# Performance work log

Hardware: AMD Instinct MI355X
Metric: run time of the kernel (lower is better)

The kernel has to match this reference:

```python
import jax, jax.numpy as jnp
import numpy as np

N_NODES = 100000
N_EDGES = 1600000
NEG_SLOPE = 0.2  # PyG GATConv default


def setup_inputs() -> dict:
    key = jax.random.key(0)
    ks = jax.random.split(key, 10)
    return {
        "x": jax.random.normal(ks[0], (N_NODES, 128), dtype=jnp.float32),
        "edge_index": jax.random.randint(ks[1], (2, N_EDGES), 0, N_NODES, dtype=jnp.int64),
        "W1": jax.random.normal(ks[2], (128, 128), dtype=jnp.float32) * 0.1,
        "a_src1": jax.random.normal(ks[3], (4, 32), dtype=jnp.float32) * 0.1,
        "a_dst1": jax.random.normal(ks[4], (4, 32), dtype=jnp.float32) * 0.1,
        "b1": jax.random.normal(ks[5], (128,), dtype=jnp.float32) * 0.1,
        "W2": jax.random.normal(ks[6], (128, 16), dtype=jnp.float32) * 0.1,
        "a_src2": jax.random.normal(ks[7], (1, 16), dtype=jnp.float32) * 0.1,
        "a_dst2": jax.random.normal(ks[8], (1, 16), dtype=jnp.float32) * 0.1,
        "b2": jax.random.normal(ks[9], (16,), dtype=jnp.float32) * 0.1,
    }


def _gat_layer(x, src, dst, W, a_src, a_dst, b, heads):
    # PyG GATConv (concat=True): xw -> per-edge attention -> segment softmax over
    # incoming edges of each target node -> weighted scatter-sum.
    N = x.shape[0]
    H = heads
    C = W.shape[1] // H
    xw = (x @ W).reshape(N, H, C)                      # [N,H,C]
    al = (xw * a_src).sum(-1)                          # [N,H] source term
    ar = (xw * a_dst).sum(-1)                          # [N,H] target term
    e = jax.nn.leaky_relu(al[src] + ar[dst], NEG_SLOPE)  # [E',H]
    emax = jax.ops.segment_max(e, dst, num_segments=N)   # [N,H]
    em = jnp.exp(e - emax[dst])
    denom = jax.ops.segment_sum(em, dst, num_segments=N)
    alpha = em / denom[dst]                            # [E',H]
    out = jax.ops.segment_sum(xw[src] * alpha[:, :, None], dst, num_segments=N)
    return out.reshape(N, H * C) + b


def reference(x, edge_index, W1, a_src1, a_dst1, b1, W2, a_src2, a_dst2, b2):
    N = x.shape[0]
    loop = jnp.arange(N, dtype=edge_index.dtype)
    # PyG GATConv add_self_loops=True
    src = jnp.concatenate([edge_index[0], loop])
    dst = jnp.concatenate([edge_index[1], loop])
    h = jax.nn.relu(_gat_layer(x, src, dst, W1, a_src1, a_dst1, b1, 4))
    # F.dropout(p=0.5, training=self.training): identity in eval mode
    return _gat_layer(h, src, dst, W2, a_src2, a_dst2, b2, 1)
```

## Files before the change

kernel.cpp:

```cpp
#include <hip/hip_runtime.h>
#include <hip/hip_fp16.h>

#define N_NODES 100000
#define N_EDGES 1600000
#define E_TOT   (N_EDGES + N_NODES)
#define NEG_SLOPE 0.2f
#define PART_EPB 4096
#define BSTRIDE 18432

__global__ __launch_bounds__(256)
void k_part(const int* __restrict__ ei, int* __restrict__ bcnt, int* __restrict__ pairs) {
    const int t = threadIdx.x;
    const int base = blockIdx.x * PART_EPB;
    __shared__ int lcnt[128];
    __shared__ int lbase[128];
    if (t < 128) lcnt[t] = 0;
    __syncthreads();
    int sr[16], dr[16];
#pragma unroll
    for (int u = 0; u < 16; ++u) {
        const int e = base + u * 256 + t;
        if (e < E_TOT) {
            int s, d;
            if (e < N_EDGES) { s = ei[e]; d = ei[N_EDGES + e]; }
            else             { s = d = e - N_EDGES; }
            sr[u] = s; dr[u] = d;
            atomicAdd(&lcnt[d >> 10], 1);
        } else dr[u] = -1;
    }
    __syncthreads();
    if (t < 128) {
        const int c = lcnt[t];
        lbase[t] = (c > 0) ? atomicAdd(&bcnt[t], c) : 0;
        lcnt[t] = 0;
    }
    __syncthreads();
#pragma unroll
    for (int u = 0; u < 16; ++u) {
        if (dr[u] >= 0) {
            const int bk = dr[u] >> 10;
            const int r = atomicAdd(&lcnt[bk], 1);
            pairs[(size_t)bk * BSTRIDE + lbase[bk] + r] = (sr[u] << 10) | (dr[u] & 1023);
        }
    }
}

__global__ __launch_bounds__(1024)
void k_fill3(const int* __restrict__ pairs, const int* __restrict__ bcnt,
             int* __restrict__ ioff, int* __restrict__ deg, int* __restrict__ ssrc) {
    const int bucket = blockIdx.x;
    const int t = threadIdx.x;
    const int cnt = bcnt[bucket];
    __shared__ int lhist[1024];
    __shared__ int lcur[1024];
    __shared__ int wsum[16];
    __shared__ int sbase;
    lhist[t] = 0;
    if (t == 0) {
        int b = 0;
        for (int k = 0; k < bucket; ++k) b += bcnt[k];
        sbase = b;
    }
    __syncthreads();
    for (int i = t; i < cnt; i += 1024) {
        const int p = pairs[(size_t)bucket * BSTRIDE + i];
        atomicAdd(&lhist[p & 1023], 1);
    }
    __syncthreads();
    const int v = lhist[t];
    int inc = v;
    const int lane = t & 63, wid = t >> 6;
#pragma unroll
    for (int o = 1; o < 64; o <<= 1) {
        const int nv = __shfl_up(inc, o, 64);
        if (lane >= o) inc += nv;
    }
    if (lane == 63) wsum[wid] = inc;
    __syncthreads();
    if (t == 0) {
        int acc = 0;
#pragma unroll
        for (int k = 0; k < 16; ++k) { const int tv = wsum[k]; wsum[k] = acc; acc += tv; }
    }
    __syncthreads();
    const int gofs = sbase + (inc - v) + wsum[wid];
    const int d = bucket * 1024 + t;
    if (d < N_NODES) { ioff[d] = gofs; deg[d] = v; }
    lcur[t] = gofs;
    __syncthreads();
    for (int i = t; i < cnt; i += 1024) {
        const int p = pairs[(size_t)bucket * BSTRIDE + i];
        const int pos = atomicAdd(&lcur[p & 1023], 1);
        ssrc[pos] = p >> 10;
    }
}

__global__ __launch_bounds__(256)
void k_gemm1(const float* __restrict__ x, const float* __restrict__ W1,
             const float* __restrict__ a_src1, const float* __restrict__ a_dst1,
             __half* __restrict__ xw1h, float* __restrict__ al1, float* __restrict__ ar1) {
    const int t = threadIdx.x;
    const int n0 = blockIdx.x * 32;
    __shared__ float sx[32][128];
    __shared__ float sW[32][128];

    {
        const float4* xg = (const float4*)(x + (size_t)n0 * 128);
#pragma unroll
        for (int i = 0; i < 4; ++i) {
            const int f = t + i * 256;
            ((float4*)sx)[f] = xg[f];
        }
    }

    const int tj = t & 31;
    const int tn = (t >> 5) * 4;
    float4 acc[4] = {{0,0,0,0},{0,0,0,0},{0,0,0,0},{0,0,0,0}};

    for (int kt = 0; kt < 128; kt += 32) {
        __syncthreads();
        const float4* wg = (const float4*)(W1 + (size_t)kt * 128);
#pragma unroll
        for (int i = 0; i < 4; ++i) {
            const int f = t + i * 256;
            ((float4*)sW)[f] = wg[f];
        }
        __syncthreads();
        for (int k = 0; k < 32; k += 4) {
            float4 xv[4];
#pragma unroll
            for (int i = 0; i < 4; ++i)
                xv[i] = *(const float4*)&sx[tn + i][kt + k];
#pragma unroll
            for (int kk = 0; kk < 4; ++kk) {
                const float4 wv = *(const float4*)&sW[k + kk][tj * 4];
#pragma unroll
                for (int i = 0; i < 4; ++i) {
                    const float xs = ((const float*)&xv[i])[kk];
                    acc[i].x = fmaf(xs, wv.x, acc[i].x);
                    acc[i].y = fmaf(xs, wv.y, acc[i].y);
                    acc[i].z = fmaf(xs, wv.z, acc[i].z);
                    acc[i].w = fmaf(xs, wv.w, acc[i].w);
                }
            }
        }
    }

#pragma unroll
    for (int i = 0; i < 4; ++i) {
        __half hp[4];
        hp[0] = __float2half(acc[i].x);
        hp[1] = __float2half(acc[i].y);
        hp[2] = __float2half(acc[i].z);
        hp[3] = __float2half(acc[i].w);
        *(uint2*)&xw1h[(size_t)(n0 + tn + i) * 128 + tj * 4] = *(uint2*)hp;
    }

    const float4 asv = ((const float4*)a_src1)[tj];
    const float4 adv = ((const float4*)a_dst1)[tj];
#pragma unroll
    for (int i = 0; i < 4; ++i) {
        float ps = acc[i].x * asv.x + acc[i].y * asv.y + acc[i].z * asv.z + acc[i].w * asv.w;
        float pd = acc[i].x * adv.x + acc[i].y * adv.y + acc[i].z * adv.z + acc[i].w * adv.w;
#pragma unroll
        for (int o = 1; o < 8; o <<= 1) { ps += __shfl_xor(ps, o, 64); pd += __shfl_xor(pd, o, 64); }
        if ((tj & 7) == 0) {
            const int h = tj >> 3;
            al1[(size_t)(n0 + tn + i) * 4 + h] = ps;
            ar1[(size_t)(n0 + tn + i) * 4 + h] = pd;
        }
    }
}

__global__ __launch_bounds__(256)
void k_aggr1(const int* __restrict__ ssrc, const int* __restrict__ offs,
             const int* __restrict__ deg, const float* __restrict__ al1,
             const float* __restrict__ ar1, const __half* __restrict__ xw1h,
             const float* __restrict__ b1, __half* __restrict__ out1h) {
    const int lane = threadIdx.x & 63;
    const int d = blockIdx.x * 4 + (threadIdx.x >> 6);
    const int g = lane >> 4;
    const int c = lane & 15;
    const int h = c >> 2;
    const int beg = offs[d];
    const int n = deg[d];
    const float arh = ar1[(size_t)d * 4 + h];
    float acc[8] = {0.f, 0.f, 0.f, 0.f, 0.f, 0.f, 0.f, 0.f};
    float dnm = 0.f;

    for (int base = 0; base < n; base += 8) {
#pragma unroll
        for (int u = 0; u < 2; ++u) {
            const int e = base + u * 4 + g;
            const bool p = e < n;
            const int s = ssrc[beg + (p ? e : 0)];
            float v = al1[(size_t)s * 4 + h] + arh;
            v = v > 0.f ? v : NEG_SLOPE * v;
            const float w = p ? __expf(v) : 0.f;
            const uint4 rv = *(const uint4*)&xw1h[(size_t)s * 128 + c * 8];
            const float2 f0 = __half22float2(*(const __half2*)&rv.x);
            const float2 f1 = __half22float2(*(const __half2*)&rv.y);
            const float2 f2 = __half22float2(*(const __half2*)&rv.z);
            const float2 f3 = __half22float2(*(const __half2*)&rv.w);
            acc[0] = fmaf(w, f0.x, acc[0]); acc[1] = fmaf(w, f0.y, acc[1]);
            acc[2] = fmaf(w, f1.x, acc[2]); acc[3] = fmaf(w, f1.y, acc[3]);
            acc[4] = fmaf(w, f2.x, acc[4]); acc[5] = fmaf(w, f2.y, acc[5]);
            acc[6] = fmaf(w, f3.x, acc[6]); acc[7] = fmaf(w, f3.y, acc[7]);
            dnm += w;
        }
    }
#pragma unroll
    for (int i = 0; i < 8; ++i) {
        acc[i] += __shfl_xor(acc[i], 16, 64);
        acc[i] += __shfl_xor(acc[i], 32, 64);
    }
    dnm += __shfl_xor(dnm, 16, 64);
    dnm += __shfl_xor(dnm, 32, 64);
    if (g == 0) {
        const float rc = 1.f / dnm;
        const float4 b01 = *(const float4*)&b1[c * 8];
        const float4 b23 = *(const float4*)&b1[c * 8 + 4];
        const float bb[8] = {b01.x, b01.y, b01.z, b01.w, b23.x, b23.y, b23.z, b23.w};
        __half ho[8];
#pragma unroll
        for (int i = 0; i < 8; ++i) {
            const float hv = acc[i] * rc + bb[i];
            ho[i] = __float2half(hv > 0.f ? hv : 0.f);
        }
        *(uint4*)&out1h[(size_t)d * 128 + c * 8] = *(uint4*)ho;
    }
}

__global__ __launch_bounds__(256)
void k_gemm2(const __half* __restrict__ out1h, const float* __restrict__ W2,
             const float* __restrict__ a_src2, const float* __restrict__ a_dst2,
             __half* __restrict__ xw2h, float* __restrict__ al2, float* __restrict__ ar2) {
    const int t = threadIdx.x;
    const int node0 = blockIdx.x * 16;
    __shared__ float sW[128 * 16];
    __shared__ float sh[16][129];
    for (int i = t; i < 2048; i += 256) sW[i] = W2[i];
    for (int i = t; i < 2048; i += 256) {
        const int nn = i >> 7, kk = i & 127;
        sh[nn][kk] = __half2float(out1h[(size_t)(node0 + nn) * 128 + kk]);
    }
    __syncthreads();
    const int nn = t >> 4;
    const int j = t & 15;
    float acc = 0.f;
#pragma unroll 8
    for (int k = 0; k < 128; ++k)
        acc = fmaf(sh[nn][k], sW[k * 16 + j], acc);
    xw2h[(size_t)(node0 + nn) * 16 + j] = __float2half(acc);

    float ps = acc * a_src2[j];
    float pd = acc * a_dst2[j];
#pragma unroll
    for (int o = 8; o; o >>= 1) { ps += __shfl_xor(ps, o, 64); pd += __shfl_xor(pd, o, 64); }
    if (j == 0) { al2[node0 + nn] = ps; ar2[node0 + nn] = pd; }
}

__global__ __launch_bounds__(256)
void k_aggr2(const int* __restrict__ ssrc, const int* __restrict__ offs,
             const int* __restrict__ deg, const float* __restrict__ al2,
             const float* __restrict__ ar2, const __half* __restrict__ xw2h,
             const float* __restrict__ b2, float* __restrict__ out) {
    const int lane = threadIdx.x & 63;
    const int node = blockIdx.x * 4 + (threadIdx.x >> 6);
    const int j2 = lane & 7;
    const int eL = lane >> 3;
    const int beg = offs[node];
    const int n = deg[node];
    const float ard = ar2[node];
    float a0 = 0.f, a1 = 0.f, dnm = 0.f;
    for (int base = 0; base < n; base += 16) {
#pragma unroll
        for (int u = 0; u < 2; ++u) {
            const int e = base + u * 8 + eL;
            const bool p = e < n;
            const int s = ssrc[beg + (p ? e : 0)];
            float v = al2[s] + ard;
            v = v > 0.f ? v : NEG_SLOPE * v;
            const float w = p ? __expf(v) : 0.f;
            const float2 f = __half22float2(*(const __half2*)&xw2h[(size_t)s * 16 + j2 * 2]);
            a0 = fmaf(w, f.x, a0);
            a1 = fmaf(w, f.y, a1);
            dnm += w;
        }
    }
#pragma unroll
    for (int o = 8; o < 64; o <<= 1) {
        a0 += __shfl_xor(a0, o, 64);
        a1 += __shfl_xor(a1, o, 64);
        dnm += __shfl_xor(dnm, o, 64);
    }
    if (eL == 0) {
        out[(size_t)node * 16 + j2 * 2]     = a0 / dnm + b2[j2 * 2];
        out[(size_t)node * 16 + j2 * 2 + 1] = a1 / dnm + b2[j2 * 2 + 1];
    }
}

extern "C" void kernel_launch(void* const* d_in, const int* in_sizes, int n_in,
                              void* d_out, int out_size, void* d_ws, size_t ws_size,
                              hipStream_t stream) {
    const float* x      = (const float*)d_in[0];
    const int*   ei     = (const int*)d_in[1];
    const float* W1     = (const float*)d_in[2];
    const float* a_src1 = (const float*)d_in[3];
    const float* a_dst1 = (const float*)d_in[4];
    const float* b1     = (const float*)d_in[5];
    const float* W2     = (const float*)d_in[6];
    const float* a_src2 = (const float*)d_in[7];
    const float* a_dst2 = (const float*)d_in[8];
    const float* b2     = (const float*)d_in[9];
    float* out = (float*)d_out;

    char* wsb = (char*)d_ws;
    __half* xw1h = (__half*)wsb;
    __half* xw2h = (__half*)wsb;
    float*  al2  = (float*)(wsb + (size_t)N_NODES * 16 * 2);
    float*  ar2  = al2 + N_NODES;
    __half* out1h = (__half*)(wsb + (size_t)N_NODES * 128 * 2);
    int*    pairs = (int*)out1h;
    float*  al1  = (float*)(wsb + (size_t)N_NODES * 128 * 4);
    float*  ar1  = al1 + (size_t)N_NODES * 4;
    int* ibcnt = (int*)(ar1 + (size_t)N_NODES * 4);
    int* ioff  = ibcnt + 128;
    int* ideg  = ioff + N_NODES;
    int* isrc  = ideg + N_NODES;

    hipMemsetAsync(ibcnt, 0, 128 * sizeof(int), stream);

    k_part<<<(E_TOT + PART_EPB - 1) / PART_EPB, 256, 0, stream>>>(ei, ibcnt, pairs);
    k_fill3<<<128, 1024, 0, stream>>>(pairs, ibcnt, ioff, ideg, isrc);

    k_gemm1<<<N_NODES / 32, 256, 0, stream>>>(x, W1, a_src1, a_dst1, xw1h, al1, ar1);
    k_aggr1<<<N_NODES / 4, 256, 0, stream>>>(isrc, ioff, ideg, al1, ar1, xw1h, b1, out1h);

    k_gemm2<<<N_NODES / 16, 256, 0, stream>>>(out1h, W2, a_src2, a_dst2, xw2h, al2, ar2);
    k_aggr2<<<N_NODES / 4, 256, 0, stream>>>(isrc, ioff, ideg, al2, ar2, xw2h, b2, out);
}
```

Baseline: 355.4 us.

## Fuse layer-1 GEMM with edge partitioning and use fp16 MFMA

Merges the edge-partition kernel and the layer-1 projection GEMM into one launch, with block ranges split between the two tasks so they run side by side. The GEMM moves from an LDS-tiled fp32 FMA loop to fp16 MFMA 16x16x32 instructions, loading x and W1 straight from global memory and converting them to half in registers. This removes a kernel launch and the FMA-bound GEMM time, but rounds the GEMM inputs to fp16 and reads W1 with strided scalar loads.

```diff
diff --git a/kernel.cpp b/kernel.cpp
--- a/kernel.cpp
+++ b/kernel.cpp
@@ -7,40 +7,119 @@
 #define NEG_SLOPE 0.2f
 #define PART_EPB 4096
 #define BSTRIDE 18432
+#define NGEMM (N_NODES / 32)
+#define NPART ((E_TOT + PART_EPB - 1) / PART_EPB)
+
+using f16x8 = __attribute__((ext_vector_type(8))) _Float16;
+using f32x4 = __attribute__((ext_vector_type(4))) float;
+union H8 { f16x8 v; _Float16 h[8]; };
 
 __global__ __launch_bounds__(256)
-void k_part(const int* __restrict__ ei, int* __restrict__ bcnt, int* __restrict__ pairs) {
-    const int t = threadIdx.x;
-    const int base = blockIdx.x * PART_EPB;
+void k_gemm1_part(const float* __restrict__ x, const float* __restrict__ W1,
+                  const float* __restrict__ a_src1, const float* __restrict__ a_dst1,
+                  const int* __restrict__ ei, int* __restrict__ bcnt, int* __restrict__ pairs,
+                  __half* __restrict__ xw1h, float* __restrict__ al1, float* __restrict__ ar1) {
     __shared__ int lcnt[128];
     __shared__ int lbase[128];
-    if (t < 128) lcnt[t] = 0;
-    __syncthreads();
-    int sr[16], dr[16];
-#pragma unroll
-    for (int u = 0; u < 16; ++u) {
-        const int e = base + u * 256 + t;
-        if (e < E_TOT) {
-            int s, d;
-            if (e < N_EDGES) { s = ei[e]; d = ei[N_EDGES + e]; }
-            else             { s = d = e - N_EDGES; }
-            sr[u] = s; dr[u] = d;
-            atomicAdd(&lcnt[d >> 10], 1);
-        } else dr[u] = -1;
-    }
-    __syncthreads();
-    if (t < 128) {
-        const int c = lcnt[t];
-        lbase[t] = (c > 0) ? atomicAdd(&bcnt[t], c) : 0;
-        lcnt[t] = 0;
-    }
-    __syncthreads();
-#pragma unroll
-    for (int u = 0; u < 16; ++u) {
-        if (dr[u] >= 0) {
-            const int bk = dr[u] >> 10;
-            const int r = atomicAdd(&lcnt[bk], 1);
-            pairs[(size_t)bk * BSTRIDE + lbase[bk] + r] = (sr[u] << 10) | (dr[u] & 1023);
+    const int t = threadIdx.x;
+
+    if (blockIdx.x >= NGEMM) {
+        const int base = ((int)blockIdx.x - NGEMM) * PART_EPB;
+        if (t < 128) lcnt[t] = 0;
+        __syncthreads();
+        int sr[16], dr[16];
+#pragma unroll
+        for (int u = 0; u < 16; ++u) {
+            const int e = base + u * 256 + t;
+            if (e < E_TOT) {
+                int s, d;
+                if (e < N_EDGES) { s = ei[e]; d = ei[N_EDGES + e]; }
+                else             { s = d = e - N_EDGES; }
+                sr[u] = s; dr[u] = d;
+                atomicAdd(&lcnt[d >> 10], 1);
+            } else dr[u] = -1;
+        }
+        __syncthreads();
+        if (t < 128) {
+            const int c = lcnt[t];
+            lbase[t] = (c > 0) ? atomicAdd(&bcnt[t], c) : 0;
+            lcnt[t] = 0;
+        }
+        __syncthreads();
+#pragma unroll
+        for (int u = 0; u < 16; ++u) {
+            if (dr[u] >= 0) {
+                const int bk = dr[u] >> 10;
+                const int r = atomicAdd(&lcnt[bk], 1);
+                pairs[(size_t)bk * BSTRIDE + lbase[bk] + r] = (sr[u] << 10) | (dr[u] & 1023);
+            }
+        }
+        return;
+    }
+
+    const int lane = t & 63;
+    const int w = t >> 6;
+    const int q = lane >> 4;
+    const int n15 = lane & 15;
+    const int n0 = (int)blockIdx.x * 32;
+    const int j0 = (2 * w) * 16 + n15;
+    const int j1 = (2 * w + 1) * 16 + n15;
+
+    f32x4 acc00 = {0.f, 0.f, 0.f, 0.f};
+    f32x4 acc01 = acc00, acc10 = acc00, acc11 = acc00;
+
+    for (int kt = 0; kt < 4; ++kt) {
+        const int k0 = kt * 32 + q * 8;
+        H8 A0, A1, B0, B1;
+        {
+            const float4* p = (const float4*)&x[(size_t)(n0 + n15) * 128 + k0];
+            const float4 xa = p[0], xb = p[1];
+            A0.h[0] = (_Float16)xa.x; A0.h[1] = (_Float16)xa.y;
+            A0.h[2] = (_Float16)xa.z; A0.h[3] = (_Float16)xa.w;
+            A0.h[4] = (_Float16)xb.x; A0.h[5] = (_Float16)xb.y;
+            A0.h[6] = (_Float16)xb.z; A0.h[7] = (_Float16)xb.w;
+        }
+        {
+            const float4* p = (const float4*)&x[(size_t)(n0 + 16 + n15) * 128 + k0];
+            const float4 xa = p[0], xb = p[1];
+            A1.h[0] = (_Float16)xa.x; A1.h[1] = (_Float16)xa.y;
+            A1.h[2] = (_Float16)xa.z; A1.h[3] = (_Float16)xa.w;
+            A1.h[4] = (_Float16)xb.x; A1.h[5] = (_Float16)xb.y;
+            A1.h[6] = (_Float16)xb.z; A1.h[7] = (_Float16)xb.w;
+        }
+#pragma unroll
+        for (int i = 0; i < 8; ++i) {
+            B0.h[i] = (_Float16)W1[(size_t)(k0 + i) * 128 + j0];
+            B1.h[i] = (_Float16)W1[(size_t)(k0 + i) * 128 + j1];
+        }
+        acc00 = __builtin_amdgcn_mfma_f32_16x16x32_f16(A0.v, B0.v, acc00, 0, 0, 0);
+        acc01 = __builtin_amdgcn_mfma_f32_16x16x32_f16(A0.v, B1.v, acc01, 0, 0, 0);
+        acc10 = __builtin_amdgcn_mfma_f32_16x16x32_f16(A1.v, B0.v, acc10, 0, 0, 0);
+        acc11 = __builtin_amdgcn_mfma_f32_16x16x32_f16(A1.v, B1.v, acc11, 0, 0, 0);
+    }
+
+    const float as0 = a_src1[j0], as1 = a_src1[j1];
+    const float ad0 = a_dst1[j0], ad1 = a_dst1[j1];
+#pragma unroll
+    for (int ng = 0; ng < 2; ++ng) {
+        const f32x4 accA = ng ? acc10 : acc00;
+        const f32x4 accB = ng ? acc11 : acc01;
+#pragma unroll
+        for (int r = 0; r < 4; ++r) {
+            const int node = n0 + ng * 16 + q * 4 + r;
+            xw1h[(size_t)node * 128 + j0] = __float2half(accA[r]);
+            xw1h[(size_t)node * 128 + j1] = __float2half(accB[r]);
+            float ps = accA[r] * as0 + accB[r] * as1;
+            float pd = accA[r] * ad0 + accB[r] * ad1;
+#pragma unroll
+            for (int o = 1; o < 16; o <<= 1) {
+                ps += __shfl_xor(ps, o, 64);
+                pd += __shfl_xor(pd, o, 64);
+            }
+            if (n15 == 0) {
+                al1[(size_t)node * 4 + w] = ps;
+                ar1[(size_t)node * 4 + w] = pd;
+            }
         }
     }
 }
@@ -92,83 +171,6 @@
         const int p = pairs[(size_t)bucket * BSTRIDE + i];
         const int pos = atomicAdd(&lcur[p & 1023], 1);
         ssrc[pos] = p >> 10;
-    }
-}
-
-__global__ __launch_bounds__(256)
-void k_gemm1(const float* __restrict__ x, const float* __restrict__ W1,
-             const float* __restrict__ a_src1, const float* __restrict__ a_dst1,
-             __half* __restrict__ xw1h, float* __restrict__ al1, float* __restrict__ ar1) {
-    const int t = threadIdx.x;
-    const int n0 = blockIdx.x * 32;
-    __shared__ float sx[32][128];
-    __shared__ float sW[32][128];
-
-    {
-        const float4* xg = (const float4*)(x + (size_t)n0 * 128);
-#pragma unroll
-        for (int i = 0; i < 4; ++i) {
-            const int f = t + i * 256;
-            ((float4*)sx)[f] = xg[f];
-        }
-    }
-
-    const int tj = t & 31;
-    const int tn = (t >> 5) * 4;
-    float4 acc[4] = {{0,0,0,0},{0,0,0,0},{0,0,0,0},{0,0,0,0}};
-
-    for (int kt = 0; kt < 128; kt += 32) {
-        __syncthreads();
-        const float4* wg = (const float4*)(W1 + (size_t)kt * 128);
-#pragma unroll
-        for (int i = 0; i < 4; ++i) {
-            const int f = t + i * 256;
-            ((float4*)sW)[f] = wg[f];
-        }
-        __syncthreads();
-        for (int k = 0; k < 32; k += 4) {
-            float4 xv[4];
-#pragma unroll
-            for (int i = 0; i < 4; ++i)
-                xv[i] = *(const float4*)&sx[tn + i][kt + k];
-#pragma unroll
-            for (int kk = 0; kk < 4; ++kk) {
-                const float4 wv = *(const float4*)&sW[k + kk][tj * 4];
-#pragma unroll
-                for (int i = 0; i < 4; ++i) {
-                    const float xs = ((const float*)&xv[i])[kk];
-                    acc[i].x = fmaf(xs, wv.x, acc[i].x);
-                    acc[i].y = fmaf(xs, wv.y, acc[i].y);
-                    acc[i].z = fmaf(xs, wv.z, acc[i].z);
-                    acc[i].w = fmaf(xs, wv.w, acc[i].w);
-                }
-            }
-        }
-    }
-
-#pragma unroll
-    for (int i = 0; i < 4; ++i) {
-        __half hp[4];
-        hp[0] = __float2half(acc[i].x);
-        hp[1] = __float2half(acc[i].y);
-        hp[2] = __float2half(acc[i].z);
-        hp[3] = __float2half(acc[i].w);
-        *(uint2*)&xw1h[(size_t)(n0 + tn + i) * 128 + tj * 4] = *(uint2*)hp;
-    }
-
-    const float4 asv = ((const float4*)a_src1)[tj];
-    const float4 adv = ((const float4*)a_dst1)[tj];
-#pragma unroll
-    for (int i = 0; i < 4; ++i) {
-        float ps = acc[i].x * asv.x + acc[i].y * asv.y + acc[i].z * asv.z + acc[i].w * asv.w;
-        float pd = acc[i].x * adv.x + acc[i].y * adv.y + acc[i].z * adv.z + acc[i].w * adv.w;
-#pragma unroll
-        for (int o = 1; o < 8; o <<= 1) { ps += __shfl_xor(ps, o, 64); pd += __shfl_xor(pd, o, 64); }
-        if ((tj & 7) == 0) {
-            const int h = tj >> 3;
-            al1[(size_t)(n0 + tn + i) * 4 + h] = ps;
-            ar1[(size_t)(n0 + tn + i) * 4 + h] = pd;
-        }
     }
 }
 
@@ -331,10 +333,10 @@
 
     hipMemsetAsync(ibcnt, 0, 128 * sizeof(int), stream);
 
-    k_part<<<(E_TOT + PART_EPB - 1) / PART_EPB, 256, 0, stream>>>(ei, ibcnt, pairs);
+    k_gemm1_part<<<NGEMM + NPART, 256, 0, stream>>>(x, W1, a_src1, a_dst1,
+                                                    ei, ibcnt, pairs, xw1h, al1, ar1);
     k_fill3<<<128, 1024, 0, stream>>>(pairs, ibcnt, ioff, ideg, isrc);
 
-    k_gemm1<<<N_NODES / 32, 256, 0, stream>>>(x, W1, a_src1, a_dst1, xw1h, al1, ar1);
     k_aggr1<<<N_NODES / 4, 256, 0, stream>>>(isrc, ioff, ideg, al1, ar1, xw1h, b1, out1h);
 
     k_gemm2<<<N_NODES / 16, 256, 0, stream>>>(out1h, W2, a_src2, a_dst2, xw2h, al2, ar2);
```

Measured after the change: 336.0 us. -5.5%, faster.
